# Performance work log

Measured on AMD Instinct MI355X. Metric: run time of the kernel, lower is better.

The kernel has to match this reference:

```python
import jax, jax.numpy as jnp
import numpy as np

B = 5                      # dat_sz hardcoded in module; kernel shapes force batch == 5
X_DIM = 4096
H_DIM = 4096
T_DIM = 4096
D_DIM = X_DIM // T_DIM     # = 1 (required so z_dim == t_dim broadcasts in reparameterize_nm)
L_DIM = D_DIM * (D_DIM + 1) // 2
Z_DIM = T_DIM * L_DIM      # = 4096


def _linear_params(key, din, dout):
    kw, kb = jax.random.split(key)
    W = jax.random.normal(kw, (din, dout), dtype=jnp.float32) / np.float32(np.sqrt(din))
    b = jax.random.normal(kb, (dout,), dtype=jnp.float32) * np.float32(0.01)
    return W, b


def setup_inputs() -> dict:
    key = jax.random.key(0)
    ks = jax.random.split(key, 20)
    inp = {}
    inp["x"] = jax.random.normal(ks[0], (B, X_DIM), dtype=jnp.float32)
    inp["eps_xi"] = jax.random.normal(ks[1], (B, T_DIM), dtype=jnp.float32)
    inp["eps_f"] = jax.random.normal(ks[2], (B, D_DIM), dtype=jnp.float32)
    inp["eps_z"] = jax.random.normal(ks[3], (B, Z_DIM), dtype=jnp.float32)
    inp["W1"], inp["b1"] = _linear_params(ks[4], X_DIM, H_DIM)
    inp["W11"], inp["b11"] = _linear_params(ks[5], H_DIM, T_DIM)
    inp["W12"], inp["b12"] = _linear_params(ks[6], H_DIM, T_DIM)
    inp["W2"], inp["b2"] = _linear_params(ks[7], D_DIM, H_DIM)
    inp["W21"], inp["b21"] = _linear_params(ks[8], H_DIM, Z_DIM)
    inp["W22"], inp["b22"] = _linear_params(ks[9], H_DIM, T_DIM)
    inp["W23"], inp["b23"] = _linear_params(ks[10], X_DIM + Z_DIM, H_DIM)
    inp["W24"], inp["b24"] = _linear_params(ks[11], H_DIM, T_DIM + D_DIM)
    inp["W25"], inp["b25"] = _linear_params(ks[12], H_DIM, T_DIM + D_DIM)
    inp["W3"], inp["b3"] = _linear_params(ks[13], Z_DIM, H_DIM)
    inp["W31"], inp["b31"] = _linear_params(ks[14], H_DIM, X_DIM)
    inp["W32"], inp["b32"] = _linear_params(ks[15], H_DIM, X_DIM)
    inp["s"] = jax.random.normal(ks[16], (B, T_DIM), dtype=jnp.float32)
    inp["t"] = jax.random.normal(ks[17], (B, D_DIM), dtype=jnp.float32)
    inp["sigma"] = jnp.asarray(0.01, dtype=jnp.float32)
    inp["w"] = jnp.ones((T_DIM,), dtype=jnp.float32) / np.float32(T_DIM)
    inp["dist"] = 1  # unused by forward (matches torch signature)
    return inp


def _ard_kernel(a, b, sigma, w):
    # K[i,j] = sigma^2 * exp(-0.5 * sum_d w_d (a_i,d - b_j,d)^2)
    # Vectorized replacement of the original O(B^2) Python double loop.
    d2 = (a[:, None, :] - b[None, :, :]) ** 2            # [B, B, T]
    return (sigma ** 2) * jnp.exp(-0.5 * jnp.einsum('ijt,t->ij', d2, w))


def reference(x, eps_xi, eps_f, eps_z,
              W1, b1, W11, b11, W12, b12,
              W2, b2, W21, b21, W22, b22,
              W23, b23, W24, b24, W25, b25,
              W3, b3, W31, b31, W32, b32,
              s, t, sigma, w, dist):
    relu = jax.nn.relu
    # encode_1
    h1 = relu(x @ W1 + b1)
    qxi_mean = h1 @ W11 + b11
    log_qxi_cov = h1 @ W12 + b12
    # reparameterize_nm
    xi = jnp.exp(0.5 * log_qxi_cov) * eps_xi + qxi_mean
    # reparameterize_gp (training branch)
    K_ss = _ard_kernel(s, s, sigma, w)                    # [5,5]
    K_xs = _ard_kernel(xi, s, sigma, w)                   # [5,5]
    kk_inv = K_xs @ jnp.linalg.inv(K_ss)                  # [5,5]
    qf_mean = kk_inv @ t                                  # [5,D]
    cov = _ard_kernel(xi, xi, sigma, w) - kk_inv @ _ard_kernel(s, xi, sigma, w)
    qf_cov = jnp.diag(cov)                                # [5]
    f = jnp.sqrt(qf_cov)[:, None] * eps_f + qf_mean       # [5,D]
    # encode_2
    h2 = relu(f @ W2 + b2)
    z_mean = h2 @ W21 + b21                               # [5,Z]
    z_cov = h2 @ W22 + b22                                # [5,T] (== Z since d_dim=1)
    z = jnp.exp(0.5 * z_cov) * eps_z + z_mean
    # encode_3
    h23 = relu(jnp.concatenate([x, z], axis=1) @ W23 + b23)
    r_mean = h23 @ W24 + b24                              # [5,T+D]
    r_cov = h23 @ W25 + b25
    # decode
    h3 = relu(z @ W3 + b3)
    x_mean = h3 @ W31 + b31
    x_cov = h3 @ W32 + b32
    # losses
    qf_cov2 = jnp.broadcast_to(qf_cov[:, None], (B, D_DIM))
    q_mean = jnp.concatenate([qxi_mean, qf_mean], axis=1)
    q_cov = jnp.concatenate([log_qxi_cov, jnp.log(qf_cov2)], axis=1)
    kld1 = 0.5 * jnp.sum(-z_cov - 1.0 + jnp.exp(z_cov) + z_mean ** 2) / B
    kld2 = 0.5 * jnp.sum(r_cov - q_cov - 1.0
                         + jnp.exp(q_cov - r_cov)
                         + (q_mean - r_mean) ** 2 * jnp.exp(-r_cov)) / B
    kld_loss = kld1 + kld2
    log_pi = jnp.log(jnp.asarray(np.pi, dtype=jnp.float32))
    nll_loss = 0.5 * jnp.sum(log_pi + x_cov + jnp.exp(-x_cov) * (x - x_mean) ** 2) / B
    return (kld_loss, nll_loss, z_mean, z_cov, x_mean, x_cov)
```

## Files before the change

### kernel.cpp

```cpp
#include <hip/hip_runtime.h>
#include <math.h>

#define B5 5
#define DX 4096
#define DT 4096
#define DR 4097

enum {
  WS_SUMS  = 0,
  WS_CNT1  = 3,
  WS_CNT2  = 4,
  WS_ZERO_END = 8,
  WS_ACT1  = 16,
  WS_ACT23 = WS_ACT1  + 20480,
  WS_ACT3  = WS_ACT23 + 20480,
  WS_QXI_F = WS_ACT3  + 20480,
  WS_LQC_F = WS_QXI_F + 20480,
  WS_XIV   = WS_LQC_F + 20480,
  WS_Z     = WS_XIV   + 20480,
  WS_KSS   = WS_Z     + 20480,
  WS_KXS   = WS_KSS + 32,
  WS_F     = WS_KXS + 32,
  WS_QFM   = WS_F   + 8,
  WS_QFC   = WS_QFM + 8,
  WS_PART  = 143472,
  WS_P_H1  = WS_PART,
  WS_P_QXI = WS_P_H1  + 1310720,
  WS_P_LQC = WS_P_QXI + 1310720,
  WS_P_ZM  = WS_P_LQC + 1310720,
  WS_P_ZC  = WS_P_ZM  + 1310720,
  WS_P_H23 = WS_P_ZC  + 1310720,
  WS_P_H3  = WS_P_H23 + 2621440,
  WS_P_RM  = WS_P_H3  + 1310720,
  WS_P_RC  = WS_P_RM  + 1311040,
  WS_P_XM  = WS_P_RC  + 1311040,
  WS_P_XC  = WS_P_XM  + 1310720,
  WS_END   = WS_P_XC  + 1310720
};

#define GCOLS 128
#define GK    64
#define WROWS 16

__device__ inline float wave_sum(float v) {
  #pragma unroll
  for (int o = 32; o > 0; o >>= 1) v += __shfl_down(v, o, 64);
  return v;
}

template<int PROLOG, int DUAL, int ALIGNED>
__device__ __forceinline__ void gemm5_body(
    float* sx, float* red, int bx, int by,
    const float* __restrict__ p0, const float* __restrict__ p1,
    const float* __restrict__ p2,
    const float* __restrict__ Wa, const float* __restrict__ Wb,
    float* __restrict__ Pa,       float* __restrict__ Pb,
    int din, int dout)
{
  const int tid  = threadIdx.x;
  const int lane = tid & 63;
  const int wv   = tid >> 6;
  const long i0  = (long)by * GK;
  const long r0  = i0 + (long)wv * WROWS;

  float* sw = sx + wv * 80;
  for (int t = lane; t < B5 * WROWS; t += 64) {
    int b  = t >> 4;
    int il = t & 15;
    int i  = (int)(r0 + il);
    float v;
    if (PROLOG == 0)      v = p0[(long)b * din + i];
    else if (PROLOG == 2) v = fmaxf(p0[b] * p1[i] + p2[i], 0.f);
    else                  v = (i < DX) ? p0[(long)b * DX + i] : p1[(long)b * DT + (i - DX)];
    sw[t] = v;
  }

  const long o0 = (long)bx * GCOLS + lane * 2;
  const bool v0 = (o0 < dout);
  const bool v1 = (o0 + 1 < dout);

  float accA[B5][2] = {};
  float accB[B5][2] = {};
  const float* wa = Wa + r0 * dout + o0;
  const float* wb = DUAL ? (Wb + r0 * dout + o0) : nullptr;

  #pragma unroll 8
  for (int il = 0; il < WROWS; ++il) {
    float w0a, w1a, w0b = 0.f, w1b = 0.f;
    if (ALIGNED) {
      float2 ta = *(const float2*)wa; w0a = ta.x; w1a = ta.y;
      if (DUAL) { float2 tb = *(const float2*)wb; w0b = tb.x; w1b = tb.y; }
    } else {
      w0a = v0 ? wa[0] : 0.f; w1a = v1 ? wa[1] : 0.f;
      if (DUAL) { w0b = v0 ? wb[0] : 0.f; w1b = v1 ? wb[1] : 0.f; }
    }
    #pragma unroll
    for (int b = 0; b < B5; ++b) {
      float xv = sw[b * WROWS + il];
      accA[b][0] += xv * w0a; accA[b][1] += xv * w1a;
      if (DUAL) { accB[b][0] += xv * w0b; accB[b][1] += xv * w1b; }
    }
    wa += dout; if (DUAL) wb += dout;
  }

  const int NJ = DUAL ? 20 : 10;
  if (wv > 0) {
    float* rr = red + (long)(wv - 1) * NJ * 64 + lane;
    #pragma unroll
    for (int b = 0; b < B5; ++b) {
      rr[(b*2)*64] = accA[b][0]; rr[(b*2+1)*64] = accA[b][1];
      if (DUAL) { rr[(10+b*2)*64] = accB[b][0]; rr[(10+b*2+1)*64] = accB[b][1]; }
    }
  }
  __syncthreads();
  if (wv == 0) {
    #pragma unroll
    for (int w2 = 0; w2 < 3; ++w2) {
      const float* rr = red + (long)w2 * NJ * 64 + lane;
      #pragma unroll
      for (int b = 0; b < B5; ++b) {
        accA[b][0] += rr[(b*2)*64]; accA[b][1] += rr[(b*2+1)*64];
        if (DUAL) { accB[b][0] += rr[(10+b*2)*64]; accB[b][1] += rr[(10+b*2+1)*64]; }
      }
    }
    if (v0) {
      #pragma unroll
      for (int b = 0; b < B5; ++b) {
        float* pa = Pa + ((long)by * B5 + b) * dout + o0;
        if (ALIGNED) *(float2*)pa = make_float2(accA[b][0], accA[b][1]);
        else { pa[0] = accA[b][0]; if (v1) pa[1] = accA[b][1]; }
        if (DUAL) {
          float* pb = Pb + ((long)by * B5 + b) * dout + o0;
          if (ALIGNED) *(float2*)pb = make_float2(accB[b][0], accB[b][1]);
          else { pb[0] = accB[b][0]; if (v1) pb[1] = accB[b][1]; }
        }
      }
    }
  }
}

template<int PROLOG, int DUAL, int ALIGNED>
__global__ __launch_bounds__(256) void gemm5(
    const float* __restrict__ p0, const float* __restrict__ p1,
    const float* __restrict__ p2,
    const float* __restrict__ Wa, const float* __restrict__ Wb,
    float* __restrict__ Pa,       float* __restrict__ Pb,
    int din, int dout)
{
  __shared__ float sx[4 * 80];
  __shared__ float red[3 * 20 * 64];
  gemm5_body<PROLOG, DUAL, ALIGNED>(sx, red, blockIdx.x, blockIdx.y,
      p0, p1, p2, Wa, Wb, Pa, Pb, din, dout);
}

__global__ __launch_bounds__(256) void gemm5_G46(
    const float* __restrict__ x,   const float* __restrict__ z,
    const float* __restrict__ W23, float* __restrict__ P23,
    const float* __restrict__ W3,  float* __restrict__ P3)
{
  __shared__ float sx[4 * 80];
  __shared__ float red[3 * 20 * 64];
  int id = blockIdx.x;
  if (id < 4096) {
    gemm5_body<3, 0, 1>(sx, red, id & 31, id >> 5, x, z, nullptr,
                        W23, nullptr, P23, nullptr, 8192, 4096);
  } else {
    id -= 4096;
    gemm5_body<0, 0, 1>(sx, red, id & 31, id >> 5, z, nullptr, nullptr,
                        W3, nullptr, P3, nullptr, 4096, 4096);
  }
}

__global__ __launch_bounds__(256) void gemm5_G57(
    const float* __restrict__ act23,
    const float* __restrict__ W24, const float* __restrict__ W25,
    float* __restrict__ PRM,       float* __restrict__ PRC,
    const float* __restrict__ act3,
    const float* __restrict__ W31, const float* __restrict__ W32,
    float* __restrict__ PXM,       float* __restrict__ PXC)
{
  __shared__ float sx[4 * 80];
  __shared__ float red[3 * 20 * 64];
  int id = blockIdx.x;
  if (id < 2112) {
    gemm5_body<0, 1, 0>(sx, red, id % 33, id / 33, act23, nullptr, nullptr,
                        W24, W25, PRM, PRC, 4096, 4097);
  } else {
    id -= 2112;
    gemm5_body<0, 1, 1>(sx, red, id & 31, id >> 5, act3, nullptr, nullptr,
                        W31, W32, PXM, PXC, 4096, 4096);
  }
}

__global__ __launch_bounds__(256) void k_act1(
    const float* __restrict__ P, const float* __restrict__ bias, float* __restrict__ act,
    float* __restrict__ ctrl)
{
  if (blockIdx.x == 0 && threadIdx.x < WS_ZERO_END) ctrl[threadIdx.x] = 0.f;
  int idx = blockIdx.x * 256 + threadIdx.x;
  int b = idx >> 12, col = idx & (DT - 1);
  const float* pp = P + (long)b * DT + col;
  float s = 0.f;
  #pragma unroll 8
  for (int ks = 0; ks < 64; ++ks) s += pp[(long)ks * (B5 * DT)];
  act[idx] = fmaxf(s + bias[col], 0.f);
}

__global__ __launch_bounds__(256) void k_act23(
    const float* __restrict__ P23, const float* __restrict__ b23, float* __restrict__ act23,
    const float* __restrict__ P3,  const float* __restrict__ b3,  float* __restrict__ act3)
{
  int idx = blockIdx.x * 256 + threadIdx.x;
  if (idx < B5 * DT) {
    int b = idx >> 12, col = idx & (DT - 1);
    const float* pp = P23 + (long)b * DT + col;
    float s = 0.f;
    #pragma unroll 8
    for (int ks = 0; ks < 128; ++ks) s += pp[(long)ks * (B5 * DT)];
    act23[idx] = fmaxf(s + b23[col], 0.f);
  } else {
    int j = idx - B5 * DT;
    int b = j >> 12, col = j & (DT - 1);
    const float* pp = P3 + (long)b * DT + col;
    float s = 0.f;
    #pragma unroll 8
    for (int ks = 0; ks < 64; ++ks) s += pp[(long)ks * (B5 * DT)];
    act3[j] = fmaxf(s + b3[col], 0.f);
  }
}

__global__ __launch_bounds__(256) void k_xi(
    const float* __restrict__ Pq, const float* __restrict__ Pl,
    const float* __restrict__ b11, const float* __restrict__ b12,
    const float* __restrict__ eps_xi,
    float* __restrict__ qf, float* __restrict__ lf, float* __restrict__ xiv)
{
  int idx = blockIdx.x * 256 + threadIdx.x;
  if (idx >= B5 * DT) return;
  int b = idx >> 12, col = idx & (DT - 1);
  const float* pq = Pq + (long)b * DT + col;
  const float* pl = Pl + (long)b * DT + col;
  float sq = 0.f, sl = 0.f;
  #pragma unroll 8
  for (int ks = 0; ks < 64; ++ks) { sq += pq[(long)ks * (B5 * DT)]; sl += pl[(long)ks * (B5 * DT)]; }
  float qm = sq + b11[col];
  float lq = sl + b12[col];
  qf[idx] = qm; lf[idx] = lq;
  xiv[idx] = expf(0.5f * lq) * eps_xi[idx] + qm;
}

__global__ __launch_bounds__(256) void k_ardgp(
    const float* __restrict__ s,    const float* __restrict__ xiv,
    const float* __restrict__ w,    const float* __restrict__ sigma,
    const float* __restrict__ t_in, const float* __restrict__ eps_f,
    float* __restrict__ Kss, float* __restrict__ Kxs, int* __restrict__ cnt,
    float* __restrict__ fv, float* __restrict__ qfm, float* __restrict__ qfc)
{
  const int bid = blockIdx.x;
  const bool xs = (bid >= 25);
  int q = xs ? bid - 25 : bid;
  const int i = q / 5, j = q % 5;
  const float* aa = xs ? (xiv + (long)i * DT) : (s + (long)i * DT);
  const float* bb = s + (long)j * DT;

  float sum = 0.f;
  for (int t = threadIdx.x; t < DT; t += 256) {
    float d = aa[t] - bb[t];
    sum += w[t] * d * d;
  }
  sum = wave_sum(sum);
  __shared__ float red[4];
  int lane = threadIdx.x & 63, wv = threadIdx.x >> 6;
  if (lane == 0) red[wv] = sum;
  __syncthreads();

  if (threadIdx.x == 0) {
    float tot = red[0] + red[1] + red[2] + red[3];
    float sg = sigma[0];
    float K = sg * sg * expf(-0.5f * tot);
    (xs ? Kxs : Kss)[i * 5 + j] = K;
    __threadfence();
    int old = atomicAdd(cnt, 1);
    if (old == 49) {
      __threadfence();
      double M[5][5], Inv[5][5];
      for (int a = 0; a < 5; ++a)
        for (int b = 0; b < 5; ++b) { M[a][b] = Kss[a * 5 + b]; Inv[a][b] = (a == b) ? 1.0 : 0.0; }
      for (int c = 0; c < 5; ++c) {
        int p = c; double best = fabs(M[c][c]);
        for (int r = c + 1; r < 5; ++r) if (fabs(M[r][c]) > best) { best = fabs(M[r][c]); p = r; }
        if (p != c)
          for (int k = 0; k < 5; ++k) {
            double tm = M[c][k]; M[c][k] = M[p][k]; M[p][k] = tm;
            tm = Inv[c][k]; Inv[c][k] = Inv[p][k]; Inv[p][k] = tm;
          }
        double piv = 1.0 / M[c][c];
        for (int k = 0; k < 5; ++k) { M[c][k] *= piv; Inv[c][k] *= piv; }
        for (int r = 0; r < 5; ++r) if (r != c) {
          double m = M[r][c];
          for (int k = 0; k < 5; ++k) { M[r][k] -= m * M[c][k]; Inv[r][k] -= m * Inv[c][k]; }
        }
      }
      double kk[5][5];
      for (int a = 0; a < 5; ++a)
        for (int b = 0; b < 5; ++b) {
          double acc = 0.0;
          for (int k = 0; k < 5; ++k) acc += (double)Kxs[a * 5 + k] * Inv[k][b];
          kk[a][b] = acc;
        }
      double sg2 = (double)sg * (double)sg;
      for (int a = 0; a < 5; ++a) {
        double qm = 0.0, qc = sg2;
        for (int b = 0; b < 5; ++b) { qm += kk[a][b] * (double)t_in[b]; qc -= kk[a][b] * (double)Kxs[a * 5 + b]; }
        if (qc < 1e-12) qc = 1e-12;
        qfm[a] = (float)qm;
        qfc[a] = (float)qc;
        fv[a]  = sqrtf((float)qc) * eps_f[a] + (float)qm;
      }
    }
  }
}

__global__ __launch_bounds__(256) void k_z(
    const float* __restrict__ Pm, const float* __restrict__ Pc,
    const float* __restrict__ b21, const float* __restrict__ b22,
    const float* __restrict__ eps_z,
    float* __restrict__ out_zm, float* __restrict__ out_zc,
    float* __restrict__ zv, float* __restrict__ kld1sum)
{
  int idx = blockIdx.x * 256 + threadIdx.x;
  float term = 0.f;
  if (idx < B5 * DT) {
    int b = idx >> 12, col = idx & (DT - 1);
    const float* pm = Pm + (long)b * DT + col;
    const float* pc = Pc + (long)b * DT + col;
    float sm = 0.f, sc = 0.f;
    #pragma unroll 8
    for (int ks = 0; ks < 64; ++ks) { sm += pm[(long)ks * (B5 * DT)]; sc += pc[(long)ks * (B5 * DT)]; }
    float zm = sm + b21[col];
    float zc = sc + b22[col];
    out_zm[idx] = zm; out_zc[idx] = zc;
    zv[idx] = expf(0.5f * zc) * eps_z[idx] + zm;
    term = -zc - 1.f + expf(zc) + zm * zm;
  }
  term = wave_sum(term);
  if ((threadIdx.x & 63) == 0) atomicAdd(kld1sum, term);
}

__global__ __launch_bounds__(256) void k_fin(
    const float* __restrict__ Prm, const float* __restrict__ Prc,
    const float* __restrict__ b24, const float* __restrict__ b25,
    const float* __restrict__ qxi, const float* __restrict__ lqc,
    const float* __restrict__ qfm, const float* __restrict__ qfc,
    const float* __restrict__ Pxm, const float* __restrict__ Pxc,
    const float* __restrict__ b31, const float* __restrict__ b32,
    const float* __restrict__ x,
    float* __restrict__ out_xm, float* __restrict__ out_xc,
    float* __restrict__ sums, int* __restrict__ cnt, float* __restrict__ out01)
{
  const int gtid = blockIdx.x * 256 + threadIdx.x;
  float t2 = 0.f, t3 = 0.f;
  if (gtid < B5 * DR) {
    int b = gtid / DR, col = gtid % DR;
    const float* pm = Prm + (long)b * DR + col;
    const float* pc = Prc + (long)b * DR + col;
    float sm = 0.f, sc = 0.f;
    #pragma unroll 8
    for (int ks = 0; ks < 64; ++ks) { sm += pm[(long)ks * (B5 * DR)]; sc += pc[(long)ks * (B5 * DR)]; }
    float rm = sm + b24[col];
    float rc = sc + b25[col];
    float qm, qc;
    if (col < DT) { qm = qxi[(long)b * DT + col]; qc = lqc[(long)b * DT + col]; }
    else          { qm = qfm[b]; qc = logf(qfc[b]); }
    float d = qm - rm;
    t2 = rc - qc - 1.f + expf(qc - rc) + d * d * expf(-rc);
  } else {
    int idx = gtid - B5 * DR;
    if (idx < B5 * DX) {
      int b = idx >> 12, col = idx & (DX - 1);
      const float* pm = Pxm + (long)b * DX + col;
      const float* pc = Pxc + (long)b * DX + col;
      float sm = 0.f, sc = 0.f;
      #pragma unroll 8
      for (int ks = 0; ks < 64; ++ks) { sm += pm[(long)ks * (B5 * DX)]; sc += pc[(long)ks * (B5 * DX)]; }
      float xm = sm + b31[col];
      float xc = sc + b32[col];
      out_xm[idx] = xm; out_xc[idx] = xc;
      float d = x[idx] - xm;
      t3 = 1.14472988584940017f + xc + expf(-xc) * d * d;
    }
  }
  t2 = wave_sum(t2);
  t3 = wave_sum(t3);
  if ((threadIdx.x & 63) == 0) {
    if (t2 != 0.f) atomicAdd(&sums[1], t2);
    if (t3 != 0.f) atomicAdd(&sums[2], t3);
  }
  __syncthreads();
  if (threadIdx.x == 0) {
    __threadfence();
    int old = atomicAdd(cnt, 1);
    if (old == (int)gridDim.x - 1) {
      __threadfence();
      out01[0] = 0.5f * (sums[0] + sums[1]) / (float)B5;
      out01[1] = 0.5f * sums[2] / (float)B5;
    }
  }
}

extern "C" void kernel_launch(void* const* d_in, const int* in_sizes, int n_in,
                              void* d_out, int out_size, void* d_ws, size_t ws_size,
                              hipStream_t stream)
{
  const float* x      = (const float*)d_in[0];
  const float* eps_xi = (const float*)d_in[1];
  const float* eps_f  = (const float*)d_in[2];
  const float* eps_z  = (const float*)d_in[3];
  const float* W1  = (const float*)d_in[4];  const float* b1  = (const float*)d_in[5];
  const float* W11 = (const float*)d_in[6];  const float* b11 = (const float*)d_in[7];
  const float* W12 = (const float*)d_in[8];  const float* b12 = (const float*)d_in[9];
  const float* W2  = (const float*)d_in[10]; const float* b2  = (const float*)d_in[11];
  const float* W21 = (const float*)d_in[12]; const float* b21 = (const float*)d_in[13];
  const float* W22 = (const float*)d_in[14]; const float* b22 = (const float*)d_in[15];
  const float* W23 = (const float*)d_in[16]; const float* b23 = (const float*)d_in[17];
  const float* W24 = (const float*)d_in[18]; const float* b24 = (const float*)d_in[19];
  const float* W25 = (const float*)d_in[20]; const float* b25 = (const float*)d_in[21];
  const float* W3  = (const float*)d_in[22]; const float* b3  = (const float*)d_in[23];
  const float* W31 = (const float*)d_in[24]; const float* b31 = (const float*)d_in[25];
  const float* W32 = (const float*)d_in[26]; const float* b32 = (const float*)d_in[27];
  const float* s     = (const float*)d_in[28];
  const float* t     = (const float*)d_in[29];
  const float* sigma = (const float*)d_in[30];
  const float* w     = (const float*)d_in[31];

  float* ws  = (float*)d_ws;
  float* out = (float*)d_out;

  dim3 blk(256);

  gemm5<0,0,1><<<dim3(32,64), blk, 0, stream>>>(
      x, nullptr, nullptr, W1, nullptr, ws + WS_P_H1, nullptr, 4096, 4096);
  k_act1<<<80, blk, 0, stream>>>(ws + WS_P_H1, b1, ws + WS_ACT1, ws);
  gemm5<0,1,1><<<dim3(32,64), blk, 0, stream>>>(
      ws + WS_ACT1, nullptr, nullptr, W11, W12, ws + WS_P_QXI, ws + WS_P_LQC, 4096, 4096);
  k_xi<<<80, blk, 0, stream>>>(
      ws + WS_P_QXI, ws + WS_P_LQC, b11, b12, eps_xi,
      ws + WS_QXI_F, ws + WS_LQC_F, ws + WS_XIV);
  k_ardgp<<<50, blk, 0, stream>>>(
      s, ws + WS_XIV, w, sigma, t, eps_f,
      ws + WS_KSS, ws + WS_KXS, (int*)(ws + WS_CNT1),
      ws + WS_F, ws + WS_QFM, ws + WS_QFC);
  gemm5<2,1,1><<<dim3(32,64), blk, 0, stream>>>(
      ws + WS_F, W2, b2, W21, W22, ws + WS_P_ZM, ws + WS_P_ZC, 4096, 4096);
  k_z<<<80, blk, 0, stream>>>(
      ws + WS_P_ZM, ws + WS_P_ZC, b21, b22, eps_z,
      out + 2, out + 2 + 20480, ws + WS_Z, ws + WS_SUMS);
  gemm5_G46<<<6144, blk, 0, stream>>>(
      x, ws + WS_Z, W23, ws + WS_P_H23, W3, ws + WS_P_H3);
  k_act23<<<160, blk, 0, stream>>>(
      ws + WS_P_H23, b23, ws + WS_ACT23, ws + WS_P_H3, b3, ws + WS_ACT3);
  gemm5_G57<<<4160, blk, 0, stream>>>(
      ws + WS_ACT23, W24, W25, ws + WS_P_RM, ws + WS_P_RC,
      ws + WS_ACT3,  W31, W32, ws + WS_P_XM, ws + WS_P_XC);
  k_fin<<<161, blk, 0, stream>>>(
      ws + WS_P_RM, ws + WS_P_RC, b24, b25,
      ws + WS_QXI_F, ws + WS_LQC_F,
      ws + WS_QFM, ws + WS_QFC,
      ws + WS_P_XM, ws + WS_P_XC, b31, b32, x,
      out + 2 + 40960, out + 2 + 61440,
      ws + WS_SUMS, (int*)(ws + WS_CNT2), out);
}
```

Measured before the change: 242.0 us.

## Widen GEMM column tiles to float4 and fuse xi reduction with ARD kernel

Each lane of the skinny batch-5 GEMM now computes four output columns with float4 weight loads instead of two with float2, which halves the grid size and doubles the register accumulators and shared reduction buffer. Separately, the xi reduction kernel and the ARD-GP kernel are merged into one launch. The cross-covariance blocks spin on an atomic counter until all xi blocks finish, while the s-s blocks proceed immediately. This removes one kernel launch and aims for wider memory transactions, at the risk of more register pressure, lower occupancy and a spin-wait that relies on all 130 blocks being co-resident.

```diff
diff --git a/kernel.cpp b/kernel.cpp
--- a/kernel.cpp
+++ b/kernel.cpp
@@ -8,8 +8,9 @@
 
 enum {
   WS_SUMS  = 0,
-  WS_CNT1  = 3,
-  WS_CNT2  = 4,
+  WS_CNT_XI  = 3,
+  WS_CNT_FIN = 4,
+  WS_CNT_ARD = 5,
   WS_ZERO_END = 8,
   WS_ACT1  = 16,
   WS_ACT23 = WS_ACT1  + 20480,
@@ -38,7 +39,7 @@
   WS_END   = WS_P_XC  + 1310720
 };
 
-#define GCOLS 128
+#define GCOLS 256
 #define GK    64
 #define WROWS 16
 
@@ -75,42 +76,51 @@
     sw[t] = v;
   }
 
-  const long o0 = (long)bx * GCOLS + lane * 2;
-  const bool v0 = (o0 < dout);
-  const bool v1 = (o0 + 1 < dout);
-
-  float accA[B5][2] = {};
-  float accB[B5][2] = {};
+  const long o0 = (long)bx * GCOLS + lane * 4;
+  const bool c0 = (o0 < dout), c1 = (o0 + 1 < dout), c2 = (o0 + 2 < dout), c3 = (o0 + 3 < dout);
+
+  float accA[B5][4] = {};
+  float accB[B5][4] = {};
   const float* wa = Wa + r0 * dout + o0;
   const float* wb = DUAL ? (Wb + r0 * dout + o0) : nullptr;
 
   #pragma unroll 8
   for (int il = 0; il < WROWS; ++il) {
-    float w0a, w1a, w0b = 0.f, w1b = 0.f;
+    float4 A, Bv;
     if (ALIGNED) {
-      float2 ta = *(const float2*)wa; w0a = ta.x; w1a = ta.y;
-      if (DUAL) { float2 tb = *(const float2*)wb; w0b = tb.x; w1b = tb.y; }
+      A = *(const float4*)wa;
+      if (DUAL) Bv = *(const float4*)wb;
     } else {
-      w0a = v0 ? wa[0] : 0.f; w1a = v1 ? wa[1] : 0.f;
-      if (DUAL) { w0b = v0 ? wb[0] : 0.f; w1b = v1 ? wb[1] : 0.f; }
+      A.x = c0 ? wa[0] : 0.f; A.y = c1 ? wa[1] : 0.f;
+      A.z = c2 ? wa[2] : 0.f; A.w = c3 ? wa[3] : 0.f;
+      if (DUAL) {
+        Bv.x = c0 ? wb[0] : 0.f; Bv.y = c1 ? wb[1] : 0.f;
+        Bv.z = c2 ? wb[2] : 0.f; Bv.w = c3 ? wb[3] : 0.f;
+      }
     }
     #pragma unroll
     for (int b = 0; b < B5; ++b) {
       float xv = sw[b * WROWS + il];
-      accA[b][0] += xv * w0a; accA[b][1] += xv * w1a;
-      if (DUAL) { accB[b][0] += xv * w0b; accB[b][1] += xv * w1b; }
+      accA[b][0] += xv * A.x;  accA[b][1] += xv * A.y;
+      accA[b][2] += xv * A.z;  accA[b][3] += xv * A.w;
+      if (DUAL) {
+        accB[b][0] += xv * Bv.x; accB[b][1] += xv * Bv.y;
+        accB[b][2] += xv * Bv.z; accB[b][3] += xv * Bv.w;
+      }
     }
     wa += dout; if (DUAL) wb += dout;
   }
 
-  const int NJ = DUAL ? 20 : 10;
+  const int NJ = DUAL ? 40 : 20;
   if (wv > 0) {
     float* rr = red + (long)(wv - 1) * NJ * 64 + lane;
     #pragma unroll
-    for (int b = 0; b < B5; ++b) {
-      rr[(b*2)*64] = accA[b][0]; rr[(b*2+1)*64] = accA[b][1];
-      if (DUAL) { rr[(10+b*2)*64] = accB[b][0]; rr[(10+b*2+1)*64] = accB[b][1]; }
-    }
+    for (int b = 0; b < B5; ++b)
+      #pragma unroll
+      for (int j = 0; j < 4; ++j) {
+        rr[(b*4+j)*64] = accA[b][j];
+        if (DUAL) rr[(20+b*4+j)*64] = accB[b][j];
+      }
   }
   __syncthreads();
   if (wv == 0) {
@@ -118,21 +128,25 @@
     for (int w2 = 0; w2 < 3; ++w2) {
       const float* rr = red + (long)w2 * NJ * 64 + lane;
       #pragma unroll
-      for (int b = 0; b < B5; ++b) {
-        accA[b][0] += rr[(b*2)*64]; accA[b][1] += rr[(b*2+1)*64];
-        if (DUAL) { accB[b][0] += rr[(10+b*2)*64]; accB[b][1] += rr[(10+b*2+1)*64]; }
-      }
-    }
-    if (v0) {
+      for (int b = 0; b < B5; ++b)
+        #pragma unroll
+        for (int j = 0; j < 4; ++j) {
+          accA[b][j] += rr[(b*4+j)*64];
+          if (DUAL) accB[b][j] += rr[(20+b*4+j)*64];
+        }
+    }
+    if (c0) {
       #pragma unroll
       for (int b = 0; b < B5; ++b) {
         float* pa = Pa + ((long)by * B5 + b) * dout + o0;
-        if (ALIGNED) *(float2*)pa = make_float2(accA[b][0], accA[b][1]);
-        else { pa[0] = accA[b][0]; if (v1) pa[1] = accA[b][1]; }
+        if (ALIGNED) *(float4*)pa = make_float4(accA[b][0], accA[b][1], accA[b][2], accA[b][3]);
+        else { pa[0] = accA[b][0]; if (c1) pa[1] = accA[b][1];
+               if (c2) pa[2] = accA[b][2]; if (c3) pa[3] = accA[b][3]; }
         if (DUAL) {
           float* pb = Pb + ((long)by * B5 + b) * dout + o0;
-          if (ALIGNED) *(float2*)pb = make_float2(accB[b][0], accB[b][1]);
-          else { pb[0] = accB[b][0]; if (v1) pb[1] = accB[b][1]; }
+          if (ALIGNED) *(float4*)pb = make_float4(accB[b][0], accB[b][1], accB[b][2], accB[b][3]);
+          else { pb[0] = accB[b][0]; if (c1) pb[1] = accB[b][1];
+                 if (c2) pb[2] = accB[b][2]; if (c3) pb[3] = accB[b][3]; }
         }
       }
     }
@@ -148,7 +162,7 @@
     int din, int dout)
 {
   __shared__ float sx[4 * 80];
-  __shared__ float red[3 * 20 * 64];
+  __shared__ float red[3 * 40 * 64];
   gemm5_body<PROLOG, DUAL, ALIGNED>(sx, red, blockIdx.x, blockIdx.y,
       p0, p1, p2, Wa, Wb, Pa, Pb, din, dout);
 }
@@ -159,14 +173,14 @@
     const float* __restrict__ W3,  float* __restrict__ P3)
 {
   __shared__ float sx[4 * 80];
-  __shared__ float red[3 * 20 * 64];
+  __shared__ float red[3 * 40 * 64];
   int id = blockIdx.x;
-  if (id < 4096) {
-    gemm5_body<3, 0, 1>(sx, red, id & 31, id >> 5, x, z, nullptr,
+  if (id < 2048) {
+    gemm5_body<3, 0, 1>(sx, red, id & 15, id >> 4, x, z, nullptr,
                         W23, nullptr, P23, nullptr, 8192, 4096);
   } else {
-    id -= 4096;
-    gemm5_body<0, 0, 1>(sx, red, id & 31, id >> 5, z, nullptr, nullptr,
+    id -= 2048;
+    gemm5_body<0, 0, 1>(sx, red, id & 15, id >> 4, z, nullptr, nullptr,
                         W3, nullptr, P3, nullptr, 4096, 4096);
   }
 }
@@ -180,14 +194,14 @@
     float* __restrict__ PXM,       float* __restrict__ PXC)
 {
   __shared__ float sx[4 * 80];
-  __shared__ float red[3 * 20 * 64];
+  __shared__ float red[3 * 40 * 64];
   int id = blockIdx.x;
-  if (id < 2112) {
-    gemm5_body<0, 1, 0>(sx, red, id % 33, id / 33, act23, nullptr, nullptr,
+  if (id < 1088) {
+    gemm5_body<0, 1, 0>(sx, red, id % 17, id / 17, act23, nullptr, nullptr,
                         W24, W25, PRM, PRC, 4096, 4097);
   } else {
-    id -= 2112;
-    gemm5_body<0, 1, 1>(sx, red, id & 31, id >> 5, act3, nullptr, nullptr,
+    id -= 1088;
+    gemm5_body<0, 1, 1>(sx, red, id & 15, id >> 4, act3, nullptr, nullptr,
                         W31, W32, PXM, PXC, 4096, 4096);
   }
 }
@@ -229,37 +243,46 @@
   }
 }
 
-__global__ __launch_bounds__(256) void k_xi(
+__global__ __launch_bounds__(256) void k_xiard(
     const float* __restrict__ Pq, const float* __restrict__ Pl,
     const float* __restrict__ b11, const float* __restrict__ b12,
     const float* __restrict__ eps_xi,
-    float* __restrict__ qf, float* __restrict__ lf, float* __restrict__ xiv)
-{
-  int idx = blockIdx.x * 256 + threadIdx.x;
-  if (idx >= B5 * DT) return;
-  int b = idx >> 12, col = idx & (DT - 1);
-  const float* pq = Pq + (long)b * DT + col;
-  const float* pl = Pl + (long)b * DT + col;
-  float sq = 0.f, sl = 0.f;
-  #pragma unroll 8
-  for (int ks = 0; ks < 64; ++ks) { sq += pq[(long)ks * (B5 * DT)]; sl += pl[(long)ks * (B5 * DT)]; }
-  float qm = sq + b11[col];
-  float lq = sl + b12[col];
-  qf[idx] = qm; lf[idx] = lq;
-  xiv[idx] = expf(0.5f * lq) * eps_xi[idx] + qm;
-}
-
-__global__ __launch_bounds__(256) void k_ardgp(
-    const float* __restrict__ s,    const float* __restrict__ xiv,
-    const float* __restrict__ w,    const float* __restrict__ sigma,
+    const float* __restrict__ s,   const float* __restrict__ w,
+    const float* __restrict__ sigma,
     const float* __restrict__ t_in, const float* __restrict__ eps_f,
-    float* __restrict__ Kss, float* __restrict__ Kxs, int* __restrict__ cnt,
+    float* __restrict__ qf, float* __restrict__ lf, float* __restrict__ xiv,
+    float* __restrict__ Kss, float* __restrict__ Kxs,
+    int* __restrict__ cnt_xi, int* __restrict__ cnt_ard,
     float* __restrict__ fv, float* __restrict__ qfm, float* __restrict__ qfc)
 {
-  const int bid = blockIdx.x;
+  if (blockIdx.x < 80) {
+    int idx = blockIdx.x * 256 + threadIdx.x;
+    int b = idx >> 12, col = idx & (DT - 1);
+    const float* pq = Pq + (long)b * DT + col;
+    const float* pl = Pl + (long)b * DT + col;
+    float sq = 0.f, sl = 0.f;
+    #pragma unroll 8
+    for (int ks = 0; ks < 64; ++ks) { sq += pq[(long)ks * (B5 * DT)]; sl += pl[(long)ks * (B5 * DT)]; }
+    float qm = sq + b11[col];
+    float lq = sl + b12[col];
+    qf[idx] = qm; lf[idx] = lq;
+    xiv[idx] = expf(0.5f * lq) * eps_xi[idx] + qm;
+    __threadfence();
+    __syncthreads();
+    if (threadIdx.x == 0) atomicAdd(cnt_xi, 1);
+    return;
+  }
+
+  const int bid = blockIdx.x - 80;
   const bool xs = (bid >= 25);
   int q = xs ? bid - 25 : bid;
   const int i = q / 5, j = q % 5;
+
+  if (xs) {
+    if (threadIdx.x == 0) { while (atomicAdd(cnt_xi, 0) < 80) {} }
+    __syncthreads();
+    __threadfence();
+  }
   const float* aa = xs ? (xiv + (long)i * DT) : (s + (long)i * DT);
   const float* bb = s + (long)j * DT;
 
@@ -280,7 +303,7 @@
     float K = sg * sg * expf(-0.5f * tot);
     (xs ? Kxs : Kss)[i * 5 + j] = K;
     __threadfence();
-    int old = atomicAdd(cnt, 1);
+    int old = atomicAdd(cnt_ard, 1);
     if (old == 49) {
       __threadfence();
       double M[5][5], Inv[5][5];
@@ -438,28 +461,28 @@
 
   dim3 blk(256);
 
-  gemm5<0,0,1><<<dim3(32,64), blk, 0, stream>>>(
+  gemm5<0,0,1><<<dim3(16,64), blk, 0, stream>>>(
       x, nullptr, nullptr, W1, nullptr, ws + WS_P_H1, nullptr, 4096, 4096);
   k_act1<<<80, blk, 0, stream>>>(ws + WS_P_H1, b1, ws + WS_ACT1, ws);
-  gemm5<0,1,1><<<dim3(32,64), blk, 0, stream>>>(
+  gemm5<0,1,1><<<dim3(16,64), blk, 0, stream>>>(
       ws + WS_ACT1, nullptr, nullptr, W11, W12, ws + WS_P_QXI, ws + WS_P_LQC, 4096, 4096);
-  k_xi<<<80, blk, 0, stream>>>(
+  k_xiard<<<130, blk, 0, stream>>>(
       ws + WS_P_QXI, ws + WS_P_LQC, b11, b12, eps_xi,
-      ws + WS_QXI_F, ws + WS_LQC_F, ws + WS_XIV);
-  k_ardgp<<<50, blk, 0, stream>>>(
-      s, ws + WS_XIV, w, sigma, t, eps_f,
-      ws + WS_KSS, ws + WS_KXS, (int*)(ws + WS_CNT1),
+      s, w, sigma, t, eps_f,
+      ws + WS_QXI_F, ws + WS_LQC_F, ws + WS_XIV,
+      ws + WS_KSS, ws + WS_KXS,
+      (int*)(ws + WS_CNT_XI), (int*)(ws + WS_CNT_ARD),
       ws + WS_F, ws + WS_QFM, ws + WS_QFC);
-  gemm5<2,1,1><<<dim3(32,64), blk, 0, stream>>>(
+  gemm5<2,1,1><<<dim3(16,64), blk, 0, stream>>>(
       ws + WS_F, W2, b2, W21, W22, ws + WS_P_ZM, ws + WS_P_ZC, 4096, 4096);
   k_z<<<80, blk, 0, stream>>>(
       ws + WS_P_ZM, ws + WS_P_ZC, b21, b22, eps_z,
       out + 2, out + 2 + 20480, ws + WS_Z, ws + WS_SUMS);
-  gemm5_G46<<<6144, blk, 0, stream>>>(
+  gemm5_G46<<<3072, blk, 0, stream>>>(
       x, ws + WS_Z, W23, ws + WS_P_H23, W3, ws + WS_P_H3);
   k_act23<<<160, blk, 0, stream>>>(
       ws + WS_P_H23, b23, ws + WS_ACT23, ws + WS_P_H3, b3, ws + WS_ACT3);
-  gemm5_G57<<<4160, blk, 0, stream>>>(
+  gemm5_G57<<<2112, blk, 0, stream>>>(
       ws + WS_ACT23, W24, W25, ws + WS_P_RM, ws + WS_P_RC,
       ws + WS_ACT3,  W31, W32, ws + WS_P_XM, ws + WS_P_XC);
   k_fin<<<161, blk, 0, stream>>>(
@@ -468,5 +491,5 @@
       ws + WS_QFM, ws + WS_QFC,
       ws + WS_P_XM, ws + WS_P_XC, b31, b32, x,
       out + 2 + 40960, out + 2 + 61440,
-      ws + WS_SUMS, (int*)(ws + WS_CNT2), out);
-}
+      ws + WS_SUMS, (int*)(ws + WS_CNT_FIN), out);
+}
```

Measured after the change: 257.5 us. 6.4% more time.

## Double GEMV K-slice depth and fuse xi reduction with ARD kernel

Applied to the files above, without the earlier changes.

Doubles each block's K-slice (GK 64→128, 32 rows per wave), halving the GEMV grids and the partial-sum buffers and reduction loops. The xi partial reduction and the ARD-GP kernel are merged into one launch: the Kxs blocks spin-wait on an atomic counter until the 80 reduction blocks finish. This removes one launch and halves partial-sum traffic, but fewer blocks may lower occupancy. The spin-wait assumes all blocks are co-resident, which holds at 130 blocks.

```diff
diff --git a/kernel.cpp b/kernel.cpp
--- a/kernel.cpp
+++ b/kernel.cpp
@@ -8,8 +8,9 @@
 
 enum {
   WS_SUMS  = 0,
-  WS_CNT1  = 3,
-  WS_CNT2  = 4,
+  WS_CNT_XI  = 3,
+  WS_CNT_FIN = 4,
+  WS_CNT_ARD = 5,
   WS_ZERO_END = 8,
   WS_ACT1  = 16,
   WS_ACT23 = WS_ACT1  + 20480,
@@ -25,22 +26,22 @@
   WS_QFC   = WS_QFM + 8,
   WS_PART  = 143472,
   WS_P_H1  = WS_PART,
-  WS_P_QXI = WS_P_H1  + 1310720,
-  WS_P_LQC = WS_P_QXI + 1310720,
-  WS_P_ZM  = WS_P_LQC + 1310720,
-  WS_P_ZC  = WS_P_ZM  + 1310720,
-  WS_P_H23 = WS_P_ZC  + 1310720,
-  WS_P_H3  = WS_P_H23 + 2621440,
-  WS_P_RM  = WS_P_H3  + 1310720,
-  WS_P_RC  = WS_P_RM  + 1311040,
-  WS_P_XM  = WS_P_RC  + 1311040,
-  WS_P_XC  = WS_P_XM  + 1310720,
-  WS_END   = WS_P_XC  + 1310720
+  WS_P_QXI = WS_P_H1  + 655360,
+  WS_P_LQC = WS_P_QXI + 655360,
+  WS_P_ZM  = WS_P_LQC + 655360,
+  WS_P_ZC  = WS_P_ZM  + 655360,
+  WS_P_H23 = WS_P_ZC  + 655360,
+  WS_P_H3  = WS_P_H23 + 1310720,
+  WS_P_RM  = WS_P_H3  + 655360,
+  WS_P_RC  = WS_P_RM  + 655520,
+  WS_P_XM  = WS_P_RC  + 655520,
+  WS_P_XC  = WS_P_XM  + 655360,
+  WS_END   = WS_P_XC  + 655360
 };
 
 #define GCOLS 128
-#define GK    64
-#define WROWS 16
+#define GK    128
+#define WROWS 32
 
 __device__ inline float wave_sum(float v) {
   #pragma unroll
@@ -63,10 +64,10 @@
   const long i0  = (long)by * GK;
   const long r0  = i0 + (long)wv * WROWS;
 
-  float* sw = sx + wv * 80;
+  float* sw = sx + wv * (B5 * WROWS);
   for (int t = lane; t < B5 * WROWS; t += 64) {
-    int b  = t >> 4;
-    int il = t & 15;
+    int b  = t / WROWS;
+    int il = t % WROWS;
     int i  = (int)(r0 + il);
     float v;
     if (PROLOG == 0)      v = p0[(long)b * din + i];
@@ -147,7 +148,7 @@
     float* __restrict__ Pa,       float* __restrict__ Pb,
     int din, int dout)
 {
-  __shared__ float sx[4 * 80];
+  __shared__ float sx[4 * B5 * WROWS];
   __shared__ float red[3 * 20 * 64];
   gemm5_body<PROLOG, DUAL, ALIGNED>(sx, red, blockIdx.x, blockIdx.y,
       p0, p1, p2, Wa, Wb, Pa, Pb, din, dout);
@@ -158,14 +159,14 @@
     const float* __restrict__ W23, float* __restrict__ P23,
     const float* __restrict__ W3,  float* __restrict__ P3)
 {
-  __shared__ float sx[4 * 80];
+  __shared__ float sx[4 * B5 * WROWS];
   __shared__ float red[3 * 20 * 64];
   int id = blockIdx.x;
-  if (id < 4096) {
+  if (id < 2048) {
     gemm5_body<3, 0, 1>(sx, red, id & 31, id >> 5, x, z, nullptr,
                         W23, nullptr, P23, nullptr, 8192, 4096);
   } else {
-    id -= 4096;
+    id -= 2048;
     gemm5_body<0, 0, 1>(sx, red, id & 31, id >> 5, z, nullptr, nullptr,
                         W3, nullptr, P3, nullptr, 4096, 4096);
   }
@@ -179,14 +180,14 @@
     const float* __restrict__ W31, const float* __restrict__ W32,
     float* __restrict__ PXM,       float* __restrict__ PXC)
 {
-  __shared__ float sx[4 * 80];
+  __shared__ float sx[4 * B5 * WROWS];
   __shared__ float red[3 * 20 * 64];
   int id = blockIdx.x;
-  if (id < 2112) {
+  if (id < 1056) {
     gemm5_body<0, 1, 0>(sx, red, id % 33, id / 33, act23, nullptr, nullptr,
                         W24, W25, PRM, PRC, 4096, 4097);
   } else {
-    id -= 2112;
+    id -= 1056;
     gemm5_body<0, 1, 1>(sx, red, id & 31, id >> 5, act3, nullptr, nullptr,
                         W31, W32, PXM, PXC, 4096, 4096);
   }
@@ -202,7 +203,7 @@
   const float* pp = P + (long)b * DT + col;
   float s = 0.f;
   #pragma unroll 8
-  for (int ks = 0; ks < 64; ++ks) s += pp[(long)ks * (B5 * DT)];
+  for (int ks = 0; ks < 32; ++ks) s += pp[(long)ks * (B5 * DT)];
   act[idx] = fmaxf(s + bias[col], 0.f);
 }
 
@@ -216,7 +217,7 @@
     const float* pp = P23 + (long)b * DT + col;
     float s = 0.f;
     #pragma unroll 8
-    for (int ks = 0; ks < 128; ++ks) s += pp[(long)ks * (B5 * DT)];
+    for (int ks = 0; ks < 64; ++ks) s += pp[(long)ks * (B5 * DT)];
     act23[idx] = fmaxf(s + b23[col], 0.f);
   } else {
     int j = idx - B5 * DT;
@@ -224,42 +225,51 @@
     const float* pp = P3 + (long)b * DT + col;
     float s = 0.f;
     #pragma unroll 8
-    for (int ks = 0; ks < 64; ++ks) s += pp[(long)ks * (B5 * DT)];
+    for (int ks = 0; ks < 32; ++ks) s += pp[(long)ks * (B5 * DT)];
     act3[j] = fmaxf(s + b3[col], 0.f);
   }
 }
 
-__global__ __launch_bounds__(256) void k_xi(
+__global__ __launch_bounds__(256) void k_xiard(
     const float* __restrict__ Pq, const float* __restrict__ Pl,
     const float* __restrict__ b11, const float* __restrict__ b12,
     const float* __restrict__ eps_xi,
-    float* __restrict__ qf, float* __restrict__ lf, float* __restrict__ xiv)
-{
-  int idx = blockIdx.x * 256 + threadIdx.x;
-  if (idx >= B5 * DT) return;
-  int b = idx >> 12, col = idx & (DT - 1);
-  const float* pq = Pq + (long)b * DT + col;
-  const float* pl = Pl + (long)b * DT + col;
-  float sq = 0.f, sl = 0.f;
-  #pragma unroll 8
-  for (int ks = 0; ks < 64; ++ks) { sq += pq[(long)ks * (B5 * DT)]; sl += pl[(long)ks * (B5 * DT)]; }
-  float qm = sq + b11[col];
-  float lq = sl + b12[col];
-  qf[idx] = qm; lf[idx] = lq;
-  xiv[idx] = expf(0.5f * lq) * eps_xi[idx] + qm;
-}
-
-__global__ __launch_bounds__(256) void k_ardgp(
-    const float* __restrict__ s,    const float* __restrict__ xiv,
-    const float* __restrict__ w,    const float* __restrict__ sigma,
+    const float* __restrict__ s,   const float* __restrict__ w,
+    const float* __restrict__ sigma,
     const float* __restrict__ t_in, const float* __restrict__ eps_f,
-    float* __restrict__ Kss, float* __restrict__ Kxs, int* __restrict__ cnt,
+    float* __restrict__ qf, float* __restrict__ lf, float* __restrict__ xiv,
+    float* __restrict__ Kss, float* __restrict__ Kxs,
+    int* __restrict__ cnt_xi, int* __restrict__ cnt_ard,
     float* __restrict__ fv, float* __restrict__ qfm, float* __restrict__ qfc)
 {
-  const int bid = blockIdx.x;
+  if (blockIdx.x < 80) {
+    int idx = blockIdx.x * 256 + threadIdx.x;
+    int b = idx >> 12, col = idx & (DT - 1);
+    const float* pq = Pq + (long)b * DT + col;
+    const float* pl = Pl + (long)b * DT + col;
+    float sq = 0.f, sl = 0.f;
+    #pragma unroll 8
+    for (int ks = 0; ks < 32; ++ks) { sq += pq[(long)ks * (B5 * DT)]; sl += pl[(long)ks * (B5 * DT)]; }
+    float qm = sq + b11[col];
+    float lq = sl + b12[col];
+    qf[idx] = qm; lf[idx] = lq;
+    xiv[idx] = expf(0.5f * lq) * eps_xi[idx] + qm;
+    __threadfence();
+    __syncthreads();
+    if (threadIdx.x == 0) atomicAdd(cnt_xi, 1);
+    return;
+  }
+
+  const int bid = blockIdx.x - 80;
   const bool xs = (bid >= 25);
   int q = xs ? bid - 25 : bid;
   const int i = q / 5, j = q % 5;
+
+  if (xs) {
+    if (threadIdx.x == 0) { while (atomicAdd(cnt_xi, 0) < 80) {} }
+    __syncthreads();
+    __threadfence();
+  }
   const float* aa = xs ? (xiv + (long)i * DT) : (s + (long)i * DT);
   const float* bb = s + (long)j * DT;
 
@@ -280,7 +290,7 @@
     float K = sg * sg * expf(-0.5f * tot);
     (xs ? Kxs : Kss)[i * 5 + j] = K;
     __threadfence();
-    int old = atomicAdd(cnt, 1);
+    int old = atomicAdd(cnt_ard, 1);
     if (old == 49) {
       __threadfence();
       double M[5][5], Inv[5][5];
@@ -336,7 +346,7 @@
     const float* pc = Pc + (long)b * DT + col;
     float sm = 0.f, sc = 0.f;
     #pragma unroll 8
-    for (int ks = 0; ks < 64; ++ks) { sm += pm[(long)ks * (B5 * DT)]; sc += pc[(long)ks * (B5 * DT)]; }
+    for (int ks = 0; ks < 32; ++ks) { sm += pm[(long)ks * (B5 * DT)]; sc += pc[(long)ks * (B5 * DT)]; }
     float zm = sm + b21[col];
     float zc = sc + b22[col];
     out_zm[idx] = zm; out_zc[idx] = zc;
@@ -366,7 +376,7 @@
     const float* pc = Prc + (long)b * DR + col;
     float sm = 0.f, sc = 0.f;
     #pragma unroll 8
-    for (int ks = 0; ks < 64; ++ks) { sm += pm[(long)ks * (B5 * DR)]; sc += pc[(long)ks * (B5 * DR)]; }
+    for (int ks = 0; ks < 32; ++ks) { sm += pm[(long)ks * (B5 * DR)]; sc += pc[(long)ks * (B5 * DR)]; }
     float rm = sm + b24[col];
     float rc = sc + b25[col];
     float qm, qc;
@@ -382,7 +392,7 @@
       const float* pc = Pxc + (long)b * DX + col;
       float sm = 0.f, sc = 0.f;
       #pragma unroll 8
-      for (int ks = 0; ks < 64; ++ks) { sm += pm[(long)ks * (B5 * DX)]; sc += pc[(long)ks * (B5 * DX)]; }
+      for (int ks = 0; ks < 32; ++ks) { sm += pm[(long)ks * (B5 * DX)]; sc += pc[(long)ks * (B5 * DX)]; }
       float xm = sm + b31[col];
       float xc = sc + b32[col];
       out_xm[idx] = xm; out_xc[idx] = xc;
@@ -438,28 +448,28 @@
 
   dim3 blk(256);
 
-  gemm5<0,0,1><<<dim3(32,64), blk, 0, stream>>>(
+  gemm5<0,0,1><<<dim3(32,32), blk, 0, stream>>>(
       x, nullptr, nullptr, W1, nullptr, ws + WS_P_H1, nullptr, 4096, 4096);
   k_act1<<<80, blk, 0, stream>>>(ws + WS_P_H1, b1, ws + WS_ACT1, ws);
-  gemm5<0,1,1><<<dim3(32,64), blk, 0, stream>>>(
+  gemm5<0,1,1><<<dim3(32,32), blk, 0, stream>>>(
       ws + WS_ACT1, nullptr, nullptr, W11, W12, ws + WS_P_QXI, ws + WS_P_LQC, 4096, 4096);
-  k_xi<<<80, blk, 0, stream>>>(
+  k_xiard<<<130, blk, 0, stream>>>(
       ws + WS_P_QXI, ws + WS_P_LQC, b11, b12, eps_xi,
-      ws + WS_QXI_F, ws + WS_LQC_F, ws + WS_XIV);
-  k_ardgp<<<50, blk, 0, stream>>>(
-      s, ws + WS_XIV, w, sigma, t, eps_f,
-      ws + WS_KSS, ws + WS_KXS, (int*)(ws + WS_CNT1),
+      s, w, sigma, t, eps_f,
+      ws + WS_QXI_F, ws + WS_LQC_F, ws + WS_XIV,
+      ws + WS_KSS, ws + WS_KXS,
+      (int*)(ws + WS_CNT_XI), (int*)(ws + WS_CNT_ARD),
       ws + WS_F, ws + WS_QFM, ws + WS_QFC);
-  gemm5<2,1,1><<<dim3(32,64), blk, 0, stream>>>(
+  gemm5<2,1,1><<<dim3(32,32), blk, 0, stream>>>(
       ws + WS_F, W2, b2, W21, W22, ws + WS_P_ZM, ws + WS_P_ZC, 4096, 4096);
   k_z<<<80, blk, 0, stream>>>(
       ws + WS_P_ZM, ws + WS_P_ZC, b21, b22, eps_z,
       out + 2, out + 2 + 20480, ws + WS_Z, ws + WS_SUMS);
-  gemm5_G46<<<6144, blk, 0, stream>>>(
+  gemm5_G46<<<3072, blk, 0, stream>>>(
       x, ws + WS_Z, W23, ws + WS_P_H23, W3, ws + WS_P_H3);
   k_act23<<<160, blk, 0, stream>>>(
       ws + WS_P_H23, b23, ws + WS_ACT23, ws + WS_P_H3, b3, ws + WS_ACT3);
-  gemm5_G57<<<4160, blk, 0, stream>>>(
+  gemm5_G57<<<2080, blk, 0, stream>>>(
       ws + WS_ACT23, W24, W25, ws + WS_P_RM, ws + WS_P_RC,
       ws + WS_ACT3,  W31, W32, ws + WS_P_XM, ws + WS_P_XC);
   k_fin<<<161, blk, 0, stream>>>(
@@ -468,5 +478,5 @@
       ws + WS_QFM, ws + WS_QFC,
       ws + WS_P_XM, ws + WS_P_XC, b31, b32, x,
       out + 2 + 40960, out + 2 + 61440,
-      ws + WS_SUMS, (int*)(ws + WS_CNT2), out);
-}
+      ws + WS_SUMS, (int*)(ws + WS_CNT_FIN), out);
+}
```

Result: slower. 268.6 us (+11.0%).
